# Optimization experiments

Measured on AMD Instinct MI355X. Metric: run time of the kernel, lower is better.

The kernel has to match this reference:

```python
import jax, jax.numpy as jnp
import numpy as np

BANDWIDTH = 3

def _elup1(x):
    return jnp.where(x >= 0, x + 1.0, jnp.exp(x))

def setup_inputs() -> dict:
    key = jax.random.key(0)
    ks = jax.random.split(key, 12)
    B, T, lod, act_dim, K, H = 256, 256, 64, 32, 15, 60
    lsd = 2 * lod
    latent_obs = jax.random.normal(ks[0], (B, T, lod), jnp.float32)
    obs_vars = jax.random.uniform(ks[1], (B, T, lod), jnp.float32) * 0.1 + 0.01
    actions = jax.random.normal(ks[2], (B, T, act_dim), jnp.float32)
    initial_mean = jax.random.normal(ks[3], (B, lsd), jnp.float32)
    # initial covariance factors: cu = cl = 10 (config initial_state_covar), cs = 0
    initial_cov = jnp.stack([10.0 * jnp.ones((B, lod), jnp.float32),
                             10.0 * jnp.ones((B, lod), jnp.float32),
                             jnp.zeros((B, lod), jnp.float32)], 0)
    coeff_w = jax.random.normal(ks[4], (lsd, K), jnp.float32) * 0.05
    coeff_b = jnp.zeros((K,), jnp.float32)
    ctrl_w1 = jax.random.normal(ks[5], (act_dim, H), jnp.float32) * (1.0 / np.sqrt(act_dim))
    ctrl_b1 = jnp.zeros((H,), jnp.float32)
    ctrl_w2 = jax.random.normal(ks[6], (H, lsd), jnp.float32) * (1.0 / np.sqrt(H))
    ctrl_b2 = jnp.zeros((lsd,), jnp.float32)
    tm_basis = jax.random.normal(ks[7], (4, K, lod, lod), jnp.float32) * 0.05
    tcov_u = jnp.full((lod,), np.log(np.e ** 0.1 - 0.0), jnp.float32) * 0.0 - 2.0  # elup1(-2)~0.135
    tcov_l = jnp.zeros((lod,), jnp.float32) - 2.0
    obs_valid = jax.random.bernoulli(ks[8], 0.9, (B, T))
    return {"latent_obs": latent_obs, "obs_vars": obs_vars, "actions": actions,
            "initial_mean": initial_mean, "initial_cov": initial_cov,
            "coeff_w": coeff_w, "coeff_b": coeff_b,
            "ctrl_w1": ctrl_w1, "ctrl_b1": ctrl_b1, "ctrl_w2": ctrl_w2, "ctrl_b2": ctrl_b2,
            "tm_basis": tm_basis, "tcov_u": tcov_u, "tcov_l": tcov_l,
            "obs_valid": obs_valid}

def reference(latent_obs, obs_vars, actions, initial_mean, initial_cov,
              coeff_w, coeff_b, ctrl_w1, ctrl_b1, ctrl_w2, ctrl_b2,
              tm_basis, tcov_u, tcov_l, obs_valid):
    B, T, lod = latent_obs.shape
    idx = jnp.arange(lod)
    band = (jnp.abs(idx[:, None] - idx[None, :]) <= BANDWIDTH).astype(latent_obs.dtype)
    eye = jnp.eye(lod, dtype=latent_obs.dtype)
    tm_b = tm_basis * band  # (4, K, lod, lod), banded basis matrices
    tcu = _elup1(tcov_u)
    tcl = _elup1(tcov_l)

    def dadat(A, d):   # diag(A diag(d) A^T)
        return jnp.einsum('bij,bj->bi', A * A, d)

    def dadbt(A, d, Bm):  # diag(A diag(d) B^T)
        return jnp.einsum('bij,bj->bi', A * Bm, d)

    def step(carry, xs):
        pm, cu, cl, cs = carry
        act, obs, ov, valid = xs
        # --- observation update (factorized Kalman gain) ---
        denom = cu + ov
        qu = cu / denom
        ql = cs / denom
        res = obs - pm[:, :lod]
        post_mean_upd = pm + jnp.concatenate([qu * res, ql * res], -1)
        covf = 1.0 - qu
        pcu_u, pcl_u, pcs_u = covf * cu, cl - ql * cs, covf * cs
        v = valid[:, None]
        post_mean = jnp.where(v, post_mean_upd, pm)
        pcu = jnp.where(v, pcu_u, cu)
        pcl = jnp.where(v, pcl_u, cl)
        pcs = jnp.where(v, pcs_u, cs)
        # --- action-conditional locally-linear prediction ---
        coeff = jax.nn.softmax(post_mean @ coeff_w + coeff_b, axis=-1)  # (B, K)
        tms = jnp.einsum('bk,fkij->fbij', coeff, tm_b)  # (4, B, lod, lod)
        tm11 = tms[0] + eye
        tm12 = tms[1]
        tm21 = tms[2]
        tm22 = tms[3] + eye
        mu, ml = post_mean[:, :lod], post_mean[:, lod:]
        nmu = jnp.einsum('bij,bj->bi', tm11, mu) + jnp.einsum('bij,bj->bi', tm12, ml)
        nml = jnp.einsum('bij,bj->bi', tm21, mu) + jnp.einsum('bij,bj->bi', tm22, ml)
        ctrl = jax.nn.relu(act @ ctrl_w1 + ctrl_b1) @ ctrl_w2 + ctrl_b2
        npm = jnp.concatenate([nmu, nml], -1) + ctrl
        ncu = dadat(tm11, pcu) + 2.0 * dadbt(tm11, pcs, tm12) + dadat(tm12, pcl) + tcu
        ncl = dadat(tm21, pcu) + 2.0 * dadbt(tm21, pcs, tm22) + dadat(tm22, pcl) + tcl
        ncs = (dadbt(tm21, pcu, tm11) + dadbt(tm22, pcs, tm11)
               + dadbt(tm21, pcs, tm12) + dadbt(tm22, pcl, tm12))
        carry = (npm, ncu, ncl, ncs)
        ys = (post_mean, pcu, pcl, pcs, npm, ncu, ncl, ncs)
        return carry, ys

    icu, icl, ics = initial_cov[0], initial_cov[1], initial_cov[2]
    xs = (jnp.moveaxis(actions, 1, 0), jnp.moveaxis(latent_obs, 1, 0),
          jnp.moveaxis(obs_vars, 1, 0), jnp.moveaxis(obs_valid, 1, 0))
    _, ys = jax.lax.scan(step, (initial_mean, icu, icl, ics), xs)
    # time-major -> batch-major, matching torch.stack(..., 1)
    return tuple(jnp.moveaxis(y, 0, 1) for y in ys)
```

## Files before the change

### kernel.cpp

```cpp
#include <hip/hip_runtime.h>
#include <math.h>

namespace {
constexpr int B_=256, T_=256;
constexpr int NB=7;
constexpr int CH=8;
constexpr int NCH=T_/CH;

constexpr int O_W1 = 0;
constexpr int O_W2 = O_W1+32*60;
constexpr int O_B1 = O_W2+60*128;
constexpr int O_B2 = O_B1+64;
constexpr int O_TCU= O_B2+128;
constexpr int O_TCL= O_TCU+64;
constexpr int O_PM = O_TCL+64;
constexpr int O_CU = O_PM+128;
constexpr int O_CL = O_CU+64;
constexpr int O_CS = O_CL+64;
constexpr int O_MU = O_CS+64;
constexpr int O_ML = O_MU+72;
constexpr int O_PCU= O_ML+72;
constexpr int O_PCL= O_PCU+72;
constexpr int O_PCS= O_PCL+72;
constexpr int O_BND= O_PCS+72;
constexpr int O_LG = O_BND+4*7*64;
constexpr int O_OBS= O_LG+16;
constexpr int O_OV = O_OBS+CH*64;
constexpr int O_ACT= O_OV+CH*64;
constexpr int O_CT = O_ACT+CH*32;
constexpr int O_H  = O_CT+CH*128;
constexpr int O_END= O_H+CH*60;

constexpr long long NBT = (long long)B_*T_;
constexpr long long OO1 = NBT*128;
constexpr long long OO2 = OO1 + NBT*64;
constexpr long long OO3 = OO2 + NBT*64;
constexpr long long OO4 = OO3 + NBT*64;
constexpr long long OO5 = OO4 + NBT*128;
constexpr long long OO6 = OO5 + NBT*64;
constexpr long long OO7 = OO6 + NBT*64;
}

template <int CTRL>
__device__ __forceinline__ float dpp_add(float x) {
    int v = __builtin_amdgcn_update_dpp(0, __float_as_int(x), CTRL, 0xf, 0xf, false);
    return x + __int_as_float(v);
}
__device__ __forceinline__ float wave_red64(float x) {
    x = dpp_add<0xB1>(x);
    x = dpp_add<0x4E>(x);
    x = dpp_add<0x124>(x);
    x = dpp_add<0x128>(x);
    float a = __int_as_float(__builtin_amdgcn_readlane(__float_as_int(x), 16));
    float b = __int_as_float(__builtin_amdgcn_readlane(__float_as_int(x), 32));
    float c = __int_as_float(__builtin_amdgcn_readlane(__float_as_int(x), 48));
    return x + a + b + c;
}

__global__ __launch_bounds__(256, 1)
void rkn_scan_kernel(const float* __restrict__ g_obs, const float* __restrict__ g_ovar,
                     const float* __restrict__ g_act, const float* __restrict__ g_im,
                     const float* __restrict__ g_icov, const float* __restrict__ g_cw,
                     const float* __restrict__ g_cb, const float* __restrict__ g_w1,
                     const float* __restrict__ g_b1, const float* __restrict__ g_w2,
                     const float* __restrict__ g_b2, const float* __restrict__ g_tmb,
                     const float* __restrict__ g_tcu, const float* __restrict__ g_tcl,
                     const int* __restrict__ g_valid, float* __restrict__ out)
{
    __shared__ __align__(16) float sm[O_END];
    __shared__ int s_val[CH];

    const int t = threadIdx.x;
    const int b = blockIdx.x;
    const int f = t >> 6;
    const int i = t & 63;

    for (int idx = t; idx < 32*60;  idx += 256) sm[O_W1+idx] = g_w1[idx];
    for (int idx = t; idx < 60*128; idx += 256) sm[O_W2+idx] = g_w2[idx];
    if (t < 60)  sm[O_B1+t] = g_b1[t];
    if (t < 128) sm[O_B2+t] = g_b2[t];
    if (t < 64) {
        float x = g_tcu[t]; sm[O_TCU+t] = (x >= 0.f) ? x + 1.f : __expf(x);
        float y = g_tcl[t]; sm[O_TCL+t] = (y >= 0.f) ? y + 1.f : __expf(y);
        sm[O_CU+t] = g_icov[0*B_*64 + b*64 + t];
        sm[O_CL+t] = g_icov[1*B_*64 + b*64 + t];
        sm[O_CS+t] = g_icov[2*B_*64 + b*64 + t];
    }
    if (t < 128) sm[O_PM+t] = g_im[b*128 + t];
    for (int idx = t; idx < 5*72; idx += 256) sm[O_MU+idx] = 0.f;

    float cwa[4], cwb[4], cbq[4];
    #pragma unroll
    for (int q = 0; q < 4; ++q) {
        int k = 4*f + q;
        bool ok = (k < 15);
        cwa[q] = ok ? g_cw[i*15 + k]      : 0.f;
        cwb[q] = ok ? g_cw[(64+i)*15 + k] : 0.f;
        cbq[q] = ok ? g_cb[k] * (1.f/64.f) : 0.f;
    }

    float bas[15][NB];
    #pragma unroll
    for (int k = 0; k < 15; ++k) {
        #pragma unroll
        for (int d = 0; d < NB; ++d) {
            int j = i - 3 + d;
            bas[k][d] = (j >= 0 && j < 64)
                ? g_tmb[(((long long)f*15 + k)*64 + i)*64 + j] : 0.f;
        }
    }

    const float* pobs = g_obs  + (size_t)b*T_*64;
    const float* pov  = g_ovar + (size_t)b*T_*64;
    const float* pact = g_act  + (size_t)b*T_*32;
    const int*   pval = g_valid + (size_t)b*T_;
    const size_t bt0  = (size_t)b*T_;

    float4 pfA = {0,0,0,0}, pfB = {0,0,0,0};
    int vpf = 0;
    {
        if (t < 128)  pfA = *(const float4*)(pobs + t*4);
        else          pfA = *(const float4*)(pov + (t-128)*4);
        if (t < 64)   pfB = *(const float4*)(pact + t*4);
        if (t >= 64 && t < 64+CH) vpf = pval[t-64];
    }

    float h0 = 0.f, h1 = 0.f;

    #pragma unroll 1
    for (int c = 0; c < NCH; ++c) {
        if (t < 128)  *(float4*)&sm[O_OBS + t*4] = pfA;
        else          *(float4*)&sm[O_OV + (t-128)*4] = pfA;
        if (t < 64)   *(float4*)&sm[O_ACT + t*4] = pfB;
        if (t >= 64 && t < 64+CH) s_val[t-64] = vpf;
        __syncthreads();

        if (c + 1 < NCH) {
            const int co = (c+1)*CH;
            if (t < 128)  pfA = *(const float4*)(pobs + co*64 + t*4);
            else          pfA = *(const float4*)(pov  + co*64 + (t-128)*4);
            if (t < 64)   pfB = *(const float4*)(pact + co*32 + t*4);
            if (t >= 64 && t < 64+CH) vpf = pval[co + t-64];
        }

        #pragma unroll 1
        for (int r = 0; r < 2; ++r) {
            int slot = t + r*256;
            int s = slot >> 6, j = slot & 63;
            if (j < 60) {
                float acc = sm[O_B1+j];
                #pragma unroll
                for (int a = 0; a < 32; ++a)
                    acc += sm[O_ACT + s*32 + a] * sm[O_W1 + a*60 + j];
                sm[O_H + s*60 + j] = fmaxf(acc, 0.f);
            }
        }
        __syncthreads();

        #pragma unroll 1
        for (int r = 0; r < 4; ++r) {
            int slot = t + r*256;
            int s = slot >> 7, ii = slot & 127;
            float acc = sm[O_B2+ii];
            #pragma unroll
            for (int j = 0; j < 60; ++j)
                acc += sm[O_H + s*60 + j] * sm[O_W2 + j*128 + ii];
            sm[O_CT + s*128 + ii] = acc;
        }
        __syncthreads();

        #pragma unroll 1
        for (int s = 0; s < CH; ++s) {
            const int tt = c*CH + s;
            const size_t bt = bt0 + tt;

            if (tt > 0) {
                const size_t bp = bt - 1;
                if (f == 0)      { out[OO4 + bp*128 + i] = h0; out[OO4 + bp*128 + 64 + i] = h1; }
                else if (f == 1)   out[OO5 + bp*64 + i] = h0;
                else if (f == 2)   out[OO7 + bp*64 + i] = h0;
                else               out[OO6 + bp*64 + i] = h0;
            }

            float cuv = sm[O_CU+i], clv = sm[O_CL+i], csv = sm[O_CS+i];
            float pmu = sm[O_PM+i], pml = sm[O_PM+64+i];
            float ob  = sm[O_OBS + s*64 + i], ovv = sm[O_OV + s*64 + i];
            const int vld = s_val[s];
            float inv = 1.f/(cuv + ovv);
            float qu = cuv*inv, ql = csv*inv;
            float res = ob - pmu;
            float covf = 1.f - qu;
            float pu  = vld ? pmu + qu*res : pmu;
            float pl  = vld ? pml + ql*res : pml;
            float pcu = vld ? covf*cuv     : cuv;
            float pcl = vld ? clv - ql*csv : clv;
            float pcs = vld ? covf*csv     : csv;

            if (f == 0)      { sm[O_MU+3+i] = pu; sm[O_ML+3+i] = pl; }
            else if (f == 1)   sm[O_PCU+3+i] = pcu;
            else if (f == 2)   sm[O_PCL+3+i] = pcl;
            else               sm[O_PCS+3+i] = pcs;

            float p0 = cbq[0] + pu*cwa[0] + pl*cwb[0];
            float p1 = cbq[1] + pu*cwa[1] + pl*cwb[1];
            float p2 = cbq[2] + pu*cwa[2] + pl*cwb[2];
            float p3 = cbq[3] + pu*cwa[3] + pl*cwb[3];
            p0 = wave_red64(p0); p1 = wave_red64(p1);
            p2 = wave_red64(p2); p3 = wave_red64(p3);
            if (i == 0) {
                sm[O_LG + 4*f + 0] = p0; sm[O_LG + 4*f + 1] = p1;
                sm[O_LG + 4*f + 2] = p2; sm[O_LG + 4*f + 3] = p3;
            }
            __syncthreads();

            if (f == 0)      { out[bt*128 + i] = pu; out[bt*128 + 64 + i] = pl; }
            else if (f == 1)   out[OO1 + bt*64 + i] = pcu;
            else if (f == 2)   out[OO2 + bt*64 + i] = pcl;
            else               out[OO3 + bt*64 + i] = pcs;

            float lgv[15];
            #pragma unroll
            for (int k = 0; k < 15; ++k) lgv[k] = sm[O_LG+k];
            float mx = lgv[0];
            #pragma unroll
            for (int k = 1; k < 15; ++k) mx = fmaxf(mx, lgv[k]);
            float ssum = 0.f;
            #pragma unroll
            for (int k = 0; k < 15; ++k) { lgv[k] = __expf(lgv[k]-mx); ssum += lgv[k]; }
            float isv = 1.f/ssum;

            float bnd[NB] = {0,0,0,0,0,0,0};
            #pragma unroll
            for (int k = 0; k < 15; ++k) {
                #pragma unroll
                for (int d = 0; d < NB; ++d) bnd[d] += lgv[k]*bas[k][d];
            }
            #pragma unroll
            for (int d = 0; d < NB; ++d) bnd[d] *= isv;
            if (f == 0 || f == 3) bnd[3] += 1.f;
            #pragma unroll
            for (int d = 0; d < NB; ++d) sm[O_BND + (f*7+d)*64 + i] = bnd[d];
            __syncthreads();

            if (f == 0) {
                float nmu = sm[O_CT + s*128 + i];
                float nml = sm[O_CT + s*128 + 64 + i];
                #pragma unroll
                for (int d = 0; d < NB; ++d) {
                    float mu_ = sm[O_MU+i+d], ml_ = sm[O_ML+i+d];
                    float Bv = sm[O_BND + (1*7+d)*64 + i];
                    float Cv = sm[O_BND + (2*7+d)*64 + i];
                    float Dv = sm[O_BND + (3*7+d)*64 + i];
                    nmu += bnd[d]*mu_ + Bv*ml_;
                    nml += Cv*mu_ + Dv*ml_;
                }
                sm[O_PM+i] = nmu; sm[O_PM+64+i] = nml;
                h0 = nmu; h1 = nml;
            } else if (f == 1) {
                float acc = sm[O_TCU+i];
                #pragma unroll
                for (int d = 0; d < NB; ++d) {
                    float Av = sm[O_BND + (0*7+d)*64 + i];
                    float Bv = bnd[d];
                    float puv = sm[O_PCU+i+d], psv = sm[O_PCS+i+d], plv = sm[O_PCL+i+d];
                    acc += Av*Av*puv + 2.f*Av*Bv*psv + Bv*Bv*plv;
                }
                sm[O_CU+i] = acc; h0 = acc;
            } else if (f == 2) {
                float acc = 0.f;
                #pragma unroll
                for (int d = 0; d < NB; ++d) {
                    float Av = sm[O_BND + (0*7+d)*64 + i];
                    float Bv = sm[O_BND + (1*7+d)*64 + i];
                    float Dv = sm[O_BND + (3*7+d)*64 + i];
                    float Cv = bnd[d];
                    float puv = sm[O_PCU+i+d], psv = sm[O_PCS+i+d], plv = sm[O_PCL+i+d];
                    acc += Av*(Cv*puv + Dv*psv) + Bv*(Cv*psv + Dv*plv);
                }
                sm[O_CS+i] = acc; h0 = acc;
            } else {
                float acc = sm[O_TCL+i];
                #pragma unroll
                for (int d = 0; d < NB; ++d) {
                    float Cv = sm[O_BND + (2*7+d)*64 + i];
                    float Dv = bnd[d];
                    float puv = sm[O_PCU+i+d], psv = sm[O_PCS+i+d], plv = sm[O_PCL+i+d];
                    acc += Cv*Cv*puv + 2.f*Cv*Dv*psv + Dv*Dv*plv;
                }
                sm[O_CL+i] = acc; h0 = acc;
            }
            __syncthreads();
        }
    }

    {
        const size_t bp = bt0 + (T_-1);
        if (f == 0)      { out[OO4 + bp*128 + i] = h0; out[OO4 + bp*128 + 64 + i] = h1; }
        else if (f == 1)   out[OO5 + bp*64 + i] = h0;
        else if (f == 2)   out[OO7 + bp*64 + i] = h0;
        else               out[OO6 + bp*64 + i] = h0;
    }
}

extern "C" void kernel_launch(void* const* d_in, const int* in_sizes, int n_in,
                              void* d_out, int out_size, void* d_ws, size_t ws_size,
                              hipStream_t stream) {
    (void)in_sizes; (void)n_in; (void)d_ws; (void)ws_size; (void)out_size;
    rkn_scan_kernel<<<B_, 256, 0, stream>>>(
        (const float*)d_in[0],  (const float*)d_in[1],  (const float*)d_in[2],
        (const float*)d_in[3],  (const float*)d_in[4],  (const float*)d_in[5],
        (const float*)d_in[6],  (const float*)d_in[7],  (const float*)d_in[8],
        (const float*)d_in[9],  (const float*)d_in[10], (const float*)d_in[11],
        (const float*)d_in[12], (const float*)d_in[13], (const int*)d_in[14],
        (float*)d_out);
}
```

Before: 711.3 us.

## Split each batch scan across 512 threads with register-held MLP weights

Doubles the block to 512 threads (8 waves), so each serial step splits the banded transition and covariance work across more waves. Each wave now holds 4 band diagonals and 2 softmax logits instead of 7 and 4. The control MLP weights move from shared memory into per-thread registers, and the MLP computation is restructured. Shared memory is repacked into interleaved float2/float4 layouts, and the cs covariance is split into two partial sums computed by different waves. Barriers become a custom waitcnt+s_barrier. The costs are more register pressure from the large weight arrays and more barrier participants per step.

```diff
diff --git a/kernel.cpp b/kernel.cpp
--- a/kernel.cpp
+++ b/kernel.cpp
@@ -2,34 +2,27 @@
 #include <math.h>
 
 namespace {
-constexpr int B_=256, T_=256;
-constexpr int NB=7;
-constexpr int CH=8;
-constexpr int NCH=T_/CH;
-
-constexpr int O_W1 = 0;
-constexpr int O_W2 = O_W1+32*60;
-constexpr int O_B1 = O_W2+60*128;
-constexpr int O_B2 = O_B1+64;
-constexpr int O_TCU= O_B2+128;
-constexpr int O_TCL= O_TCU+64;
-constexpr int O_PM = O_TCL+64;
-constexpr int O_CU = O_PM+128;
-constexpr int O_CL = O_CU+64;
-constexpr int O_CS = O_CL+64;
-constexpr int O_MU = O_CS+64;
-constexpr int O_ML = O_MU+72;
-constexpr int O_PCU= O_ML+72;
-constexpr int O_PCL= O_PCU+72;
-constexpr int O_PCS= O_PCL+72;
-constexpr int O_BND= O_PCS+72;
-constexpr int O_LG = O_BND+4*7*64;
-constexpr int O_OBS= O_LG+16;
-constexpr int O_OV = O_OBS+CH*64;
-constexpr int O_ACT= O_OV+CH*64;
-constexpr int O_CT = O_ACT+CH*32;
-constexpr int O_H  = O_CT+CH*128;
-constexpr int O_END= O_H+CH*60;
+constexpr int B_=256, T_=256, NT=512;
+constexpr int CH=8, NCH=32;
+
+constexpr int O_TCU=0;
+constexpr int O_TCL=64;
+constexpr int O_PM =128;
+constexpr int O_CU =256;
+constexpr int O_CL =320;
+constexpr int O_CS1=384;
+constexpr int O_CS2=448;
+constexpr int O_MM =512;
+constexpr int O_PA =656;
+constexpr int O_PB =800;
+constexpr int O_BND=944;
+constexpr int O_LG =2992;
+constexpr int O_OBS=3008;
+constexpr int O_OV =3520;
+constexpr int O_ACT=4032;
+constexpr int O_H  =4288;
+constexpr int O_CT =4800;
+constexpr int O_END=5824;
 
 constexpr long long NBT = (long long)B_*T_;
 constexpr long long OO1 = NBT*128;
@@ -39,6 +32,10 @@
 constexpr long long OO5 = OO4 + NBT*128;
 constexpr long long OO6 = OO5 + NBT*64;
 constexpr long long OO7 = OO6 + NBT*64;
+}
+
+__device__ __forceinline__ void bar_lds() {
+    asm volatile("s_waitcnt lgkmcnt(0)\n\ts_barrier" ::: "memory");
 }
 
 template <int CTRL>
@@ -57,7 +54,7 @@
     return x + a + b + c;
 }
 
-__global__ __launch_bounds__(256, 1)
+__global__ __launch_bounds__(NT, 2)
 void rkn_scan_kernel(const float* __restrict__ g_obs, const float* __restrict__ g_ovar,
                      const float* __restrict__ g_act, const float* __restrict__ g_im,
                      const float* __restrict__ g_icov, const float* __restrict__ g_cw,
@@ -74,39 +71,55 @@
     const int b = blockIdx.x;
     const int f = t >> 6;
     const int i = t & 63;
-
-    for (int idx = t; idx < 32*60;  idx += 256) sm[O_W1+idx] = g_w1[idx];
-    for (int idx = t; idx < 60*128; idx += 256) sm[O_W2+idx] = g_w2[idx];
-    if (t < 60)  sm[O_B1+t] = g_b1[t];
-    if (t < 128) sm[O_B2+t] = g_b2[t];
+    const int m = f >> 1;
+    const int oddw = f & 1;
+
     if (t < 64) {
         float x = g_tcu[t]; sm[O_TCU+t] = (x >= 0.f) ? x + 1.f : __expf(x);
         float y = g_tcl[t]; sm[O_TCL+t] = (y >= 0.f) ? y + 1.f : __expf(y);
-        sm[O_CU+t] = g_icov[0*B_*64 + b*64 + t];
-        sm[O_CL+t] = g_icov[1*B_*64 + b*64 + t];
-        sm[O_CS+t] = g_icov[2*B_*64 + b*64 + t];
+        sm[O_CU+t]  = g_icov[0*B_*64 + b*64 + t];
+        sm[O_CL+t]  = g_icov[1*B_*64 + b*64 + t];
+        sm[O_CS1+t] = g_icov[2*B_*64 + b*64 + t];
+        sm[O_CS2+t] = 0.f;
     }
     if (t < 128) sm[O_PM+t] = g_im[b*128 + t];
-    for (int idx = t; idx < 5*72; idx += 256) sm[O_MU+idx] = 0.f;
-
-    float cwa[4], cwb[4], cbq[4];
+    if (t < 432) sm[O_MM+t] = 0.f;
+    if (t == 0)  sm[O_LG+15] = -3.0e38f;
+
+    float w1c[32], b1r = 0.f;
+    if (i < 60) {
+        b1r = g_b1[i];
+        #pragma unroll
+        for (int a = 0; a < 32; ++a) w1c[a] = g_w1[a*60 + i];
+    } else {
+        #pragma unroll
+        for (int a = 0; a < 32; ++a) w1c[a] = 0.f;
+    }
+    const int ii2 = t & 127;
+    float w2c[60];
     #pragma unroll
-    for (int q = 0; q < 4; ++q) {
-        int k = 4*f + q;
-        bool ok = (k < 15);
-        cwa[q] = ok ? g_cw[i*15 + k]      : 0.f;
-        cwb[q] = ok ? g_cw[(64+i)*15 + k] : 0.f;
-        cbq[q] = ok ? g_cb[k] * (1.f/64.f) : 0.f;
-    }
-
-    float bas[15][NB];
+    for (int j = 0; j < 60; ++j) w2c[j] = g_w2[j*128 + ii2];
+    const float b2r = g_b2[ii2];
+
+    const int k0 = 2*f, k1 = 2*f + 1;
+    float cwa0 = g_cw[i*15 + k0], cwb0 = g_cw[(64+i)*15 + k0];
+    float cb0q = g_cb[k0] * (1.f/64.f);
+    float cwa1 = 0.f, cwb1 = 0.f, cb1q = 0.f;
+    if (k1 < 15) {
+        cwa1 = g_cw[i*15 + k1]; cwb1 = g_cw[(64+i)*15 + k1];
+        cb1q = g_cb[k1] * (1.f/64.f);
+    }
+
+    const int d0 = oddw ? 4 : 0;
+    float bas[15][4];
     #pragma unroll
     for (int k = 0; k < 15; ++k) {
         #pragma unroll
-        for (int d = 0; d < NB; ++d) {
+        for (int dd = 0; dd < 4; ++dd) {
+            int d = d0 + dd;
             int j = i - 3 + d;
-            bas[k][d] = (j >= 0 && j < 64)
-                ? g_tmb[(((long long)f*15 + k)*64 + i)*64 + j] : 0.f;
+            bas[k][dd] = (d < 7 && j >= 0 && j < 64)
+                ? g_tmb[(((long long)m*15 + k)*64 + i)*64 + j] : 0.f;
         }
     }
 
@@ -116,76 +129,64 @@
     const int*   pval = g_valid + (size_t)b*T_;
     const size_t bt0  = (size_t)b*T_;
 
-    float4 pfA = {0,0,0,0}, pfB = {0,0,0,0};
+    float4 pfA = {0,0,0,0};
     int vpf = 0;
-    {
-        if (t < 128)  pfA = *(const float4*)(pobs + t*4);
-        else          pfA = *(const float4*)(pov + (t-128)*4);
-        if (t < 64)   pfB = *(const float4*)(pact + t*4);
-        if (t >= 64 && t < 64+CH) vpf = pval[t-64];
-    }
-
-    float h0 = 0.f, h1 = 0.f;
+    if (t < 128)                  pfA = *(const float4*)(pobs + t*4);
+    else if (t < 256)             pfA = *(const float4*)(pov + (t-128)*4);
+    else if (t < 320)             pfA = *(const float4*)(pact + (t-256)*4);
+    else if (t < 328)             vpf = pval[t-320];
 
     #pragma unroll 1
     for (int c = 0; c < NCH; ++c) {
-        if (t < 128)  *(float4*)&sm[O_OBS + t*4] = pfA;
-        else          *(float4*)&sm[O_OV + (t-128)*4] = pfA;
-        if (t < 64)   *(float4*)&sm[O_ACT + t*4] = pfB;
-        if (t >= 64 && t < 64+CH) s_val[t-64] = vpf;
-        __syncthreads();
+        if (t < 128)        *(float4*)&sm[O_OBS + t*4] = pfA;
+        else if (t < 256)   *(float4*)&sm[O_OV  + (t-128)*4] = pfA;
+        else if (t < 320)   *(float4*)&sm[O_ACT + (t-256)*4] = pfA;
+        else if (t < 328)   s_val[t-320] = vpf;
+        bar_lds();
 
         if (c + 1 < NCH) {
             const int co = (c+1)*CH;
-            if (t < 128)  pfA = *(const float4*)(pobs + co*64 + t*4);
-            else          pfA = *(const float4*)(pov  + co*64 + (t-128)*4);
-            if (t < 64)   pfB = *(const float4*)(pact + co*32 + t*4);
-            if (t >= 64 && t < 64+CH) vpf = pval[co + t-64];
-        }
-
-        #pragma unroll 1
+            if (t < 128)        pfA = *(const float4*)(pobs + co*64 + t*4);
+            else if (t < 256)   pfA = *(const float4*)(pov  + co*64 + (t-128)*4);
+            else if (t < 320)   pfA = *(const float4*)(pact + co*32 + (t-256)*4);
+            else if (t < 328)   vpf = pval[co + t-320];
+        }
+
+        if (i < 60) {
+            float acc = b1r;
+            #pragma unroll
+            for (int a = 0; a < 32; ++a) acc += sm[O_ACT + f*32 + a] * w1c[a];
+            sm[O_H + f*64 + i] = fmaxf(acc, 0.f);
+        }
+        bar_lds();
+
+        #pragma unroll
         for (int r = 0; r < 2; ++r) {
-            int slot = t + r*256;
-            int s = slot >> 6, j = slot & 63;
-            if (j < 60) {
-                float acc = sm[O_B1+j];
-                #pragma unroll
-                for (int a = 0; a < 32; ++a)
-                    acc += sm[O_ACT + s*32 + a] * sm[O_W1 + a*60 + j];
-                sm[O_H + s*60 + j] = fmaxf(acc, 0.f);
-            }
-        }
-        __syncthreads();
-
-        #pragma unroll 1
-        for (int r = 0; r < 4; ++r) {
-            int slot = t + r*256;
-            int s = slot >> 7, ii = slot & 127;
-            float acc = sm[O_B2+ii];
-            #pragma unroll
-            for (int j = 0; j < 60; ++j)
-                acc += sm[O_H + s*60 + j] * sm[O_W2 + j*128 + ii];
-            sm[O_CT + s*128 + ii] = acc;
-        }
-        __syncthreads();
+            int s2 = (t >> 7) + r*4;
+            float acc = b2r;
+            #pragma unroll
+            for (int j = 0; j < 60; ++j) acc += sm[O_H + s2*64 + j] * w2c[j];
+            sm[O_CT + s2*128 + ii2] = acc;
+        }
 
         #pragma unroll 1
         for (int s = 0; s < CH; ++s) {
             const int tt = c*CH + s;
             const size_t bt = bt0 + tt;
 
+            float pmu = sm[O_PM+i], pml = sm[O_PM+64+i];
+            float cuv = sm[O_CU+i], clv = sm[O_CL+i];
+            float csv = sm[O_CS1+i] + sm[O_CS2+i];
+            float ob  = sm[O_OBS + s*64 + i], ovv = sm[O_OV + s*64 + i];
+            const int vld = s_val[s];
+
             if (tt > 0) {
                 const size_t bp = bt - 1;
-                if (f == 0)      { out[OO4 + bp*128 + i] = h0; out[OO4 + bp*128 + 64 + i] = h1; }
-                else if (f == 1)   out[OO5 + bp*64 + i] = h0;
-                else if (f == 2)   out[OO7 + bp*64 + i] = h0;
-                else               out[OO6 + bp*64 + i] = h0;
-            }
-
-            float cuv = sm[O_CU+i], clv = sm[O_CL+i], csv = sm[O_CS+i];
-            float pmu = sm[O_PM+i], pml = sm[O_PM+64+i];
-            float ob  = sm[O_OBS + s*64 + i], ovv = sm[O_OV + s*64 + i];
-            const int vld = s_val[s];
+                if (f == 3)      { out[OO4 + bp*128 + i] = pmu; out[OO4 + bp*128 + 64 + i] = pml; }
+                else if (f == 5) { out[OO5 + bp*64 + i] = cuv;  out[OO6 + bp*64 + i] = clv;
+                                   out[OO7 + bp*64 + i] = csv; }
+            }
+
             float inv = 1.f/(cuv + ovv);
             float qu = cuv*inv, ql = csv*inv;
             float res = ob - pmu;
@@ -196,31 +197,29 @@
             float pcl = vld ? clv - ql*csv : clv;
             float pcs = vld ? covf*csv     : csv;
 
-            if (f == 0)      { sm[O_MU+3+i] = pu; sm[O_ML+3+i] = pl; }
-            else if (f == 1)   sm[O_PCU+3+i] = pcu;
-            else if (f == 2)   sm[O_PCL+3+i] = pcl;
-            else               sm[O_PCS+3+i] = pcs;
-
-            float p0 = cbq[0] + pu*cwa[0] + pl*cwb[0];
-            float p1 = cbq[1] + pu*cwa[1] + pl*cwb[1];
-            float p2 = cbq[2] + pu*cwa[2] + pl*cwb[2];
-            float p3 = cbq[3] + pu*cwa[3] + pl*cwb[3];
+            if (f == 0)      { float2 v = {pu, pl};   *(float2*)&sm[O_MM + (i+3)*2] = v; }
+            else if (f == 2) { float2 v = {pcu, pcs}; *(float2*)&sm[O_PA + (i+3)*2] = v; }
+            else if (f == 4) { float2 v = {pcl, pcs}; *(float2*)&sm[O_PB + (i+3)*2] = v; }
+
+            float p0 = cb0q + pu*cwa0 + pl*cwb0;
+            float p1 = cb1q + pu*cwa1 + pl*cwb1;
             p0 = wave_red64(p0); p1 = wave_red64(p1);
-            p2 = wave_red64(p2); p3 = wave_red64(p3);
             if (i == 0) {
-                sm[O_LG + 4*f + 0] = p0; sm[O_LG + 4*f + 1] = p1;
-                sm[O_LG + 4*f + 2] = p2; sm[O_LG + 4*f + 3] = p3;
-            }
-            __syncthreads();
-
-            if (f == 0)      { out[bt*128 + i] = pu; out[bt*128 + 64 + i] = pl; }
-            else if (f == 1)   out[OO1 + bt*64 + i] = pcu;
-            else if (f == 2)   out[OO2 + bt*64 + i] = pcl;
-            else               out[OO3 + bt*64 + i] = pcs;
-
-            float lgv[15];
-            #pragma unroll
-            for (int k = 0; k < 15; ++k) lgv[k] = sm[O_LG+k];
+                sm[O_LG + k0] = p0;
+                if (k1 < 15) sm[O_LG + k1] = p1;
+            }
+            bar_lds();
+
+            if (f == 3)      { out[bt*128 + i] = pu; out[bt*128 + 64 + i] = pl; }
+            else if (f == 5) { out[OO1 + bt*64 + i] = pcu; out[OO2 + bt*64 + i] = pcl;
+                               out[OO3 + bt*64 + i] = pcs; }
+
+            float4 L0 = *(const float4*)&sm[O_LG+0];
+            float4 L1 = *(const float4*)&sm[O_LG+4];
+            float4 L2 = *(const float4*)&sm[O_LG+8];
+            float4 L3 = *(const float4*)&sm[O_LG+12];
+            float lgv[15] = {L0.x,L0.y,L0.z,L0.w, L1.x,L1.y,L1.z,L1.w,
+                             L2.x,L2.y,L2.z,L2.w, L3.x,L3.y,L3.z};
             float mx = lgv[0];
             #pragma unroll
             for (int k = 1; k < 15; ++k) mx = fmaxf(mx, lgv[k]);
@@ -229,76 +228,131 @@
             for (int k = 0; k < 15; ++k) { lgv[k] = __expf(lgv[k]-mx); ssum += lgv[k]; }
             float isv = 1.f/ssum;
 
-            float bnd[NB] = {0,0,0,0,0,0,0};
+            float bnd[4] = {0.f,0.f,0.f,0.f};
             #pragma unroll
             for (int k = 0; k < 15; ++k) {
                 #pragma unroll
-                for (int d = 0; d < NB; ++d) bnd[d] += lgv[k]*bas[k][d];
-            }
-            #pragma unroll
-            for (int d = 0; d < NB; ++d) bnd[d] *= isv;
-            if (f == 0 || f == 3) bnd[3] += 1.f;
-            #pragma unroll
-            for (int d = 0; d < NB; ++d) sm[O_BND + (f*7+d)*64 + i] = bnd[d];
-            __syncthreads();
+                for (int dd = 0; dd < 4; ++dd) bnd[dd] += lgv[k]*bas[k][dd];
+            }
+            #pragma unroll
+            for (int dd = 0; dd < 4; ++dd) bnd[dd] *= isv;
+            if (!oddw) {
+                if (f == 0 || f == 6) bnd[3] += 1.f;
+                float4 v = {bnd[0],bnd[1],bnd[2],bnd[3]};
+                *(float4*)&sm[O_BND + (m*64+i)*8] = v;
+            } else {
+                float4 v = {bnd[0],bnd[1],bnd[2],0.f};
+                *(float4*)&sm[O_BND + (m*64+i)*8 + 4] = v;
+            }
+            bar_lds();
 
             if (f == 0) {
-                float nmu = sm[O_CT + s*128 + i];
-                float nml = sm[O_CT + s*128 + 64 + i];
-                #pragma unroll
-                for (int d = 0; d < NB; ++d) {
-                    float mu_ = sm[O_MU+i+d], ml_ = sm[O_ML+i+d];
-                    float Bv = sm[O_BND + (1*7+d)*64 + i];
-                    float Cv = sm[O_BND + (2*7+d)*64 + i];
-                    float Dv = sm[O_BND + (3*7+d)*64 + i];
-                    nmu += bnd[d]*mu_ + Bv*ml_;
-                    nml += Cv*mu_ + Dv*ml_;
-                }
-                sm[O_PM+i] = nmu; sm[O_PM+64+i] = nml;
-                h0 = nmu; h1 = nml;
+                float4 a03 = *(const float4*)&sm[O_BND + (0*64+i)*8];
+                float4 a46 = *(const float4*)&sm[O_BND + (0*64+i)*8 + 4];
+                float4 b03 = *(const float4*)&sm[O_BND + (1*64+i)*8];
+                float4 b46 = *(const float4*)&sm[O_BND + (1*64+i)*8 + 4];
+                float A[7]={a03.x,a03.y,a03.z,a03.w,a46.x,a46.y,a46.z};
+                float Bb[7]={b03.x,b03.y,b03.z,b03.w,b46.x,b46.y,b46.z};
+                float acc = sm[O_CT + s*128 + i];
+                #pragma unroll
+                for (int d = 0; d < 7; ++d) {
+                    float2 mm = *(const float2*)&sm[O_MM + (i+d)*2];
+                    acc += A[d]*mm.x + Bb[d]*mm.y;
+                }
+                sm[O_PM+i] = acc;
             } else if (f == 1) {
+                float4 c03 = *(const float4*)&sm[O_BND + (2*64+i)*8];
+                float4 c46 = *(const float4*)&sm[O_BND + (2*64+i)*8 + 4];
+                float4 d03 = *(const float4*)&sm[O_BND + (3*64+i)*8];
+                float4 d46 = *(const float4*)&sm[O_BND + (3*64+i)*8 + 4];
+                float Cv[7]={c03.x,c03.y,c03.z,c03.w,c46.x,c46.y,c46.z};
+                float Dv[7]={d03.x,d03.y,d03.z,d03.w,d46.x,d46.y,d46.z};
+                float acc = sm[O_CT + s*128 + 64 + i];
+                #pragma unroll
+                for (int d = 0; d < 7; ++d) {
+                    float2 mm = *(const float2*)&sm[O_MM + (i+d)*2];
+                    acc += Cv[d]*mm.x + Dv[d]*mm.y;
+                }
+                sm[O_PM+64+i] = acc;
+            } else if (f == 2) {
+                float4 a03 = *(const float4*)&sm[O_BND + (0*64+i)*8];
+                float4 a46 = *(const float4*)&sm[O_BND + (0*64+i)*8 + 4];
+                float4 b03 = *(const float4*)&sm[O_BND + (1*64+i)*8];
+                float4 b46 = *(const float4*)&sm[O_BND + (1*64+i)*8 + 4];
+                float A[7]={a03.x,a03.y,a03.z,a03.w,a46.x,a46.y,a46.z};
+                float Bb[7]={b03.x,b03.y,b03.z,b03.w,b46.x,b46.y,b46.z};
                 float acc = sm[O_TCU+i];
                 #pragma unroll
-                for (int d = 0; d < NB; ++d) {
-                    float Av = sm[O_BND + (0*7+d)*64 + i];
-                    float Bv = bnd[d];
-                    float puv = sm[O_PCU+i+d], psv = sm[O_PCS+i+d], plv = sm[O_PCL+i+d];
-                    acc += Av*Av*puv + 2.f*Av*Bv*psv + Bv*Bv*plv;
-                }
-                sm[O_CU+i] = acc; h0 = acc;
-            } else if (f == 2) {
+                for (int d = 0; d < 7; ++d) {
+                    float2 pa = *(const float2*)&sm[O_PA + (i+d)*2];
+                    float pclv = sm[O_PB + (i+d)*2];
+                    acc += A[d]*A[d]*pa.x + 2.f*A[d]*Bb[d]*pa.y + Bb[d]*Bb[d]*pclv;
+                }
+                sm[O_CU+i] = acc;
+            } else if (f == 4) {
+                float4 c03 = *(const float4*)&sm[O_BND + (2*64+i)*8];
+                float4 c46 = *(const float4*)&sm[O_BND + (2*64+i)*8 + 4];
+                float4 d03 = *(const float4*)&sm[O_BND + (3*64+i)*8];
+                float4 d46 = *(const float4*)&sm[O_BND + (3*64+i)*8 + 4];
+                float Cv[7]={c03.x,c03.y,c03.z,c03.w,c46.x,c46.y,c46.z};
+                float Dv[7]={d03.x,d03.y,d03.z,d03.w,d46.x,d46.y,d46.z};
+                float acc = sm[O_TCL+i];
+                #pragma unroll
+                for (int d = 0; d < 7; ++d) {
+                    float2 pa = *(const float2*)&sm[O_PA + (i+d)*2];
+                    float pclv = sm[O_PB + (i+d)*2];
+                    acc += Cv[d]*Cv[d]*pa.x + 2.f*Cv[d]*Dv[d]*pa.y + Dv[d]*Dv[d]*pclv;
+                }
+                sm[O_CL+i] = acc;
+            } else if (f == 6) {
+                float4 a03 = *(const float4*)&sm[O_BND + (0*64+i)*8];
+                float4 a46 = *(const float4*)&sm[O_BND + (0*64+i)*8 + 4];
+                float4 c03 = *(const float4*)&sm[O_BND + (2*64+i)*8];
+                float4 c46 = *(const float4*)&sm[O_BND + (2*64+i)*8 + 4];
+                float4 d03 = *(const float4*)&sm[O_BND + (3*64+i)*8];
+                float4 d46 = *(const float4*)&sm[O_BND + (3*64+i)*8 + 4];
+                float A[7]={a03.x,a03.y,a03.z,a03.w,a46.x,a46.y,a46.z};
+                float Cv[7]={c03.x,c03.y,c03.z,c03.w,c46.x,c46.y,c46.z};
+                float Dv[7]={d03.x,d03.y,d03.z,d03.w,d46.x,d46.y,d46.z};
                 float acc = 0.f;
                 #pragma unroll
-                for (int d = 0; d < NB; ++d) {
-                    float Av = sm[O_BND + (0*7+d)*64 + i];
-                    float Bv = sm[O_BND + (1*7+d)*64 + i];
-                    float Dv = sm[O_BND + (3*7+d)*64 + i];
-                    float Cv = bnd[d];
-                    float puv = sm[O_PCU+i+d], psv = sm[O_PCS+i+d], plv = sm[O_PCL+i+d];
-                    acc += Av*(Cv*puv + Dv*psv) + Bv*(Cv*psv + Dv*plv);
-                }
-                sm[O_CS+i] = acc; h0 = acc;
-            } else {
-                float acc = sm[O_TCL+i];
-                #pragma unroll
-                for (int d = 0; d < NB; ++d) {
-                    float Cv = sm[O_BND + (2*7+d)*64 + i];
-                    float Dv = bnd[d];
-                    float puv = sm[O_PCU+i+d], psv = sm[O_PCS+i+d], plv = sm[O_PCL+i+d];
-                    acc += Cv*Cv*puv + 2.f*Cv*Dv*psv + Dv*Dv*plv;
-                }
-                sm[O_CL+i] = acc; h0 = acc;
-            }
-            __syncthreads();
+                for (int d = 0; d < 7; ++d) {
+                    float2 pa = *(const float2*)&sm[O_PA + (i+d)*2];
+                    acc += A[d]*(Cv[d]*pa.x + Dv[d]*pa.y);
+                }
+                sm[O_CS1+i] = acc;
+            } else if (f == 7) {
+                float4 b03 = *(const float4*)&sm[O_BND + (1*64+i)*8];
+                float4 b46 = *(const float4*)&sm[O_BND + (1*64+i)*8 + 4];
+                float4 c03 = *(const float4*)&sm[O_BND + (2*64+i)*8];
+                float4 c46 = *(const float4*)&sm[O_BND + (2*64+i)*8 + 4];
+                float4 d03 = *(const float4*)&sm[O_BND + (3*64+i)*8];
+                float4 d46 = *(const float4*)&sm[O_BND + (3*64+i)*8 + 4];
+                float Bb[7]={b03.x,b03.y,b03.z,b03.w,b46.x,b46.y,b46.z};
+                float Cv[7]={c03.x,c03.y,c03.z,c03.w,c46.x,c46.y,c46.z};
+                float Dv[7]={d03.x,d03.y,d03.z,d03.w,d46.x,d46.y,d46.z};
+                float acc = 0.f;
+                #pragma unroll
+                for (int d = 0; d < 7; ++d) {
+                    float2 pb = *(const float2*)&sm[O_PB + (i+d)*2];
+                    acc += Bb[d]*(Cv[d]*pb.y + Dv[d]*pb.x);
+                }
+                sm[O_CS2+i] = acc;
+            }
+            bar_lds();
         }
     }
 
     {
         const size_t bp = bt0 + (T_-1);
-        if (f == 0)      { out[OO4 + bp*128 + i] = h0; out[OO4 + bp*128 + 64 + i] = h1; }
-        else if (f == 1)   out[OO5 + bp*64 + i] = h0;
-        else if (f == 2)   out[OO7 + bp*64 + i] = h0;
-        else               out[OO6 + bp*64 + i] = h0;
+        if (f == 3) {
+            out[OO4 + bp*128 + i]      = sm[O_PM+i];
+            out[OO4 + bp*128 + 64 + i] = sm[O_PM+64+i];
+        } else if (f == 5) {
+            out[OO5 + bp*64 + i] = sm[O_CU+i];
+            out[OO6 + bp*64 + i] = sm[O_CL+i];
+            out[OO7 + bp*64 + i] = sm[O_CS1+i] + sm[O_CS2+i];
+        }
     }
 }
 
@@ -306,7 +360,7 @@
                               void* d_out, int out_size, void* d_ws, size_t ws_size,
                               hipStream_t stream) {
     (void)in_sizes; (void)n_in; (void)d_ws; (void)ws_size; (void)out_size;
-    rkn_scan_kernel<<<B_, 256, 0, stream>>>(
+    rkn_scan_kernel<<<B_, NT, 0, stream>>>(
         (const float*)d_in[0],  (const float*)d_in[1],  (const float*)d_in[2],
         (const float*)d_in[3],  (const float*)d_in[4],  (const float*)d_in[5],
         (const float*)d_in[6],  (const float*)d_in[7],  (const float*)d_in[8],
```

Measured after the change: 740.4 us. 4.1% more time.
